# Kernel tuning notes

Measured on AMD Instinct MI355X. Metric: run time of the kernel, lower is better.

Reference implementation:

```python
import jax, jax.numpy as jnp
import numpy as np

B, KLEN, QLEN = 4, 512, 64
KDIM = QDIM = ADIM = 512
H = 4
DK = ADIM // H


def setup_inputs() -> dict:
    key = jax.random.key(0)
    ks = jax.random.split(key, 8)
    inp = {}
    inp["key"] = jax.random.normal(ks[0], (B, KLEN, KDIM), jnp.float32)
    inp["query"] = jax.random.normal(ks[1], (B, QLEN, QDIM), jnp.float32)
    inp["mask"] = jax.random.randint(ks[2], (B, QLEN, KLEN), 0, 2, jnp.int32)
    # nn.Linear default init scale ~ 1/sqrt(fan_in)
    inp["w_key_w"] = jax.random.normal(ks[3], (ADIM, KDIM), jnp.float32) / np.sqrt(KDIM)
    inp["w_key_b"] = jnp.zeros((ADIM,), jnp.float32)
    inp["w_query_w"] = jax.random.normal(ks[4], (ADIM, QDIM), jnp.float32) / np.sqrt(QDIM)
    # weight-normed v: weight = g * v / ||v||_row, g initialized to sqrt(1/adim)
    inp["v_v"] = jax.random.normal(ks[5], (H, ADIM), jnp.float32) / np.sqrt(ADIM)
    inp["v_g"] = jnp.full((H, 1), np.sqrt(1.0 / ADIM), jnp.float32)
    inp["r"] = jnp.array([-4.0], jnp.float32)  # init_r
    return inp


def reference(key, query, mask, w_key_w, w_key_b, w_query_w, v_v, v_g, r):
    bs, klen, _ = key.shape
    qlen = query.shape[1]
    # key projection -> [B, H, klen, d_k]
    k = (jnp.einsum('bkd,ad->bka', key, w_key_w) + w_key_b)
    k = k.reshape(bs, klen, H, DK).transpose(0, 2, 1, 3)
    # query projection (no bias) -> [B, H, qlen, d_k]
    q = jnp.einsum('bqd,ad->bqa', query, w_query_w)
    q = q.reshape(bs, qlen, H, DK).transpose(0, 2, 1, 3)
    # additive energy: relu(k + q) over [B, H, qlen, klen, d_k]
    e5 = jax.nn.relu(k[:, :, None, :, :] + q[:, :, :, None, :])
    # weight-normed v linear mixes heads: Wv[n, h, d]
    Wv = (v_g * v_v / jnp.linalg.norm(v_v, axis=1, keepdims=True)).reshape(H, H, DK)
    e = jnp.einsum('bhqkd,nhd->bnqk', e5, Wv)
    e = e + r[0]
    neg_inf = jnp.finfo(e.dtype).min
    m = jnp.broadcast_to(mask[:, None, :, :], e.shape)  # [B, H, qlen, klen]
    e = jnp.where(m == 0, neg_inf, e)
    return e
```

## Files before the change

### kernel.cpp

```cpp
#include <hip/hip_runtime.h>
#include <math.h>

#define KLEN 512
#define QLEN 64
#define ADIM 512
#define BATCH 4
#define NH 4

typedef __attribute__((ext_vector_type(8))) short bf16x8;
typedef __attribute__((ext_vector_type(4))) float f32x4;
typedef _Float16 f16;
typedef __attribute__((ext_vector_type(2))) _Float16 f16x2;

__device__ __forceinline__ f16x2 u2h(unsigned int u) {
  union { unsigned int u; f16x2 h; } v; v.u = u; return v.h;
}

__device__ __forceinline__ short4 pack4(float4 x) {
  union { unsigned int u[2]; short4 s; } o;
  o.u[0] = __builtin_amdgcn_perm(__float_as_uint(x.y), __float_as_uint(x.x), 0x07060302);
  o.u[1] = __builtin_amdgcn_perm(__float_as_uint(x.w), __float_as_uint(x.z), 0x07060302);
  return o.s;
}

__global__ __launch_bounds__(512) void proj_mfma(
    const float* __restrict__ key, const float* __restrict__ query,
    const float* __restrict__ wk, const float* __restrict__ bk,
    const float* __restrict__ wq,
    const float* __restrict__ v_v, const float* __restrict__ v_g,
    f16* __restrict__ Kp, f16* __restrict__ Qp, f16* __restrict__ Wn) {
  __shared__ short At[2][64 * 40];
  __shared__ short Wt[2][64 * 40];

  const int bid = blockIdx.x;
  const int tid = threadIdx.x;

  if (bid == 288) {
    __shared__ float wred[512];
    for (int h = 0; h < NH; ++h) {
      float v0 = v_v[h * ADIM + tid];
      wred[tid] = v0 * v0;
      __syncthreads();
      for (int s2 = 256; s2 > 0; s2 >>= 1) {
        if (tid < s2) wred[tid] += wred[tid + s2];
        __syncthreads();
      }
      float scale = v_g[h] / sqrtf(wred[0]);
      Wn[h * ADIM + tid] = (f16)(v0 * scale);
      __syncthreads();
    }
    return;
  }

  const float *A, *W, *bias;
  f16* C;
  int m0, a0;
  if (bid < 256) {
    A = key; W = wk; bias = bk; C = Kp;
    m0 = (bid >> 3) * 64; a0 = (bid & 7) * 64;
  } else {
    const int t = bid - 256;
    A = query; W = wq; bias = nullptr; C = Qp;
    m0 = (t >> 3) * 64; a0 = (t & 7) * 64;
  }

  const int w = tid >> 6;
  const int wr = w >> 2;
  const int wc = w & 3;
  const int lane = tid & 63;
  const int lr = lane & 15, hi = lane >> 4;
  const int srow = tid >> 3;
  const int scol = (tid & 7) * 4;

  const float* Arow = &A[(size_t)(m0 + srow) * ADIM + scol];
  const float* Wrow = &W[(size_t)(a0 + srow) * ADIM + scol];

  f32x4 acc0 = {0.f, 0.f, 0.f, 0.f};
  f32x4 acc1 = {0.f, 0.f, 0.f, 0.f};

  {
    float4 fa = *(const float4*)&Arow[0];
    float4 fw = *(const float4*)&Wrow[0];
    *(short4*)&At[0][srow * 40 + scol] = pack4(fa);
    *(short4*)&Wt[0][srow * 40 + scol] = pack4(fw);
  }
  __syncthreads();

  for (int c = 0; c < 16; ++c) {
    float4 na, nw;
    if (c < 15) {
      na = *(const float4*)&Arow[(c + 1) * 32];
      nw = *(const float4*)&Wrow[(c + 1) * 32];
    }
    const short* Ab = At[c & 1];
    const short* Wb = Wt[c & 1];
    bf16x8 af0 = *(const bf16x8*)&Ab[(wr * 32 + lr) * 40 + hi * 8];
    bf16x8 af1 = *(const bf16x8*)&Ab[(wr * 32 + 16 + lr) * 40 + hi * 8];
    bf16x8 wf  = *(const bf16x8*)&Wb[(wc * 16 + lr) * 40 + hi * 8];
    acc0 = __builtin_amdgcn_mfma_f32_16x16x32_bf16(af0, wf, acc0, 0, 0, 0);
    acc1 = __builtin_amdgcn_mfma_f32_16x16x32_bf16(af1, wf, acc1, 0, 0, 0);
    if (c < 15) {
      *(short4*)&At[(c + 1) & 1][srow * 40 + scol] = pack4(na);
      *(short4*)&Wt[(c + 1) & 1][srow * 40 + scol] = pack4(nw);
    }
    __syncthreads();
  }

  const int ccol = a0 + wc * 16 + lr;
  const float bv = bias ? bias[ccol] : 0.f;
#pragma unroll
  for (int i = 0; i < 4; ++i) {
    const int crow0 = m0 + wr * 32 + hi * 4 + i;
    C[(size_t)crow0 * ADIM + ccol] = (f16)(acc0[i] + bv);
    C[(size_t)(crow0 + 16) * ADIM + ccol] = (f16)(acc1[i] + bv);
  }
}

__global__ __launch_bounds__(256) void energy_kernel(
    const f16* __restrict__ Kp, const f16* __restrict__ Qp,
    const f16* __restrict__ Wn, const int* __restrict__ mask,
    const float* __restrict__ r, float* __restrict__ out) {
  __shared__ f16 Kl[16 * 520];
  __shared__ f16 Ql[16 * 520];
  __shared__ float Red[2][1280];

  const int b = blockIdx.z;
  const int q0 = blockIdx.y * 16;
  const int kl0 = blockIdx.x * 16;
  const int tid = threadIdx.x;
  const int wave = tid >> 6;
  const int lane = tid & 63;
  const int klg = lane & 7;
  const int qg = lane >> 3;

  const float rv = r[0];

  const unsigned short* Kb = (const unsigned short*)(Kp + ((size_t)b * KLEN + kl0) * ADIM);
  const unsigned short* Qb = (const unsigned short*)(Qp + ((size_t)b * QLEN + q0) * ADIM);

  const unsigned int* Wd = (const unsigned int*)Wn;
  uint4 wreg = *(const uint4*)&Wd[(lane >> 4) * 256 + wave * 64 + (lane & 15) * 4];

#pragma unroll
  for (int j = 0; j < 4; ++j) {
    const int u = tid + 256 * j;
    const int row = u >> 6, c8 = (u & 63) * 8;
    *(uint4*)&Kl[row * 520 + c8] = *(const uint4*)&Kb[row * ADIM + c8];
    *(uint4*)&Ql[row * 520 + c8] = *(const uint4*)&Qb[row * ADIM + c8];
  }
  __syncthreads();

  float acc[2][2][4] = {};
  const int abase = wave * 128;

#pragma unroll
  for (int s = 0; s < 16; ++s) {
    const int off = abase + s * 8;
    uint4 ka = *(const uint4*)&Kl[klg * 520 + off];
    uint4 kb = *(const uint4*)&Kl[(klg + 8) * 520 + off];
    uint4 qa = *(const uint4*)&Ql[qg * 520 + off];
    uint4 qb = *(const uint4*)&Ql[(qg + 8) * 520 + off];
    unsigned wdw[4][4];
#pragma unroll
    for (int n = 0; n < 4; ++n) {
      wdw[n][0] = (unsigned)__builtin_amdgcn_readlane((int)wreg.x, n * 16 + s);
      wdw[n][1] = (unsigned)__builtin_amdgcn_readlane((int)wreg.y, n * 16 + s);
      wdw[n][2] = (unsigned)__builtin_amdgcn_readlane((int)wreg.z, n * 16 + s);
      wdw[n][3] = (unsigned)__builtin_amdgcn_readlane((int)wreg.w, n * 16 + s);
    }
    unsigned ks[2][4] = {{ka.x, ka.y, ka.z, ka.w}, {kb.x, kb.y, kb.z, kb.w}};
    unsigned qs[2][4] = {{qa.x, qa.y, qa.z, qa.w}, {qb.x, qb.y, qb.z, qb.w}};
#pragma unroll
    for (int j = 0; j < 4; ++j) {
      const f16x2 wv0 = u2h(wdw[0][j]), wv1 = u2h(wdw[1][j]);
      const f16x2 wv2 = u2h(wdw[2][j]), wv3 = u2h(wdw[3][j]);
#pragma unroll
      for (int ki = 0; ki < 2; ++ki) {
        const f16x2 kv = u2h(ks[ki][j]);
#pragma unroll
        for (int qi = 0; qi < 2; ++qi) {
          f16x2 sum = kv + u2h(qs[qi][j]);
          f16x2 rl = __builtin_elementwise_max(sum, (f16x2)(_Float16)0);
          acc[ki][qi][0] = __builtin_amdgcn_fdot2(rl, wv0, acc[ki][qi][0], false);
          acc[ki][qi][1] = __builtin_amdgcn_fdot2(rl, wv1, acc[ki][qi][1], false);
          acc[ki][qi][2] = __builtin_amdgcn_fdot2(rl, wv2, acc[ki][qi][2], false);
          acc[ki][qi][3] = __builtin_amdgcn_fdot2(rl, wv3, acc[ki][qi][3], false);
        }
      }
    }
  }

  const int half = wave & 1;
  if (wave < 2) {
#pragma unroll
    for (int ki = 0; ki < 2; ++ki)
#pragma unroll
      for (int qi = 0; qi < 2; ++qi) {
        const int cell = (qg + 8 * qi) * 16 + klg + 8 * ki;
#pragma unroll
        for (int n = 0; n < 4; ++n) Red[half][cell * 5 + n] = acc[ki][qi][n];
      }
  }
  __syncthreads();
  if (wave >= 2) {
#pragma unroll
    for (int ki = 0; ki < 2; ++ki)
#pragma unroll
      for (int qi = 0; qi < 2; ++qi) {
        const int cell = (qg + 8 * qi) * 16 + klg + 8 * ki;
#pragma unroll
        for (int n = 0; n < 4; ++n) Red[half][cell * 5 + n] += acc[ki][qi][n];
      }
  }
  __syncthreads();

  const float NEG_BIG = __uint_as_float(0xFF7F0000u);
  const int n = tid >> 6;
  const int q = (tid >> 2) & 15;
  const int klb = (tid & 3) * 4;
  const int4 mv = *(const int4*)&mask[((size_t)b * QLEN + q0 + q) * KLEN + kl0 + klb];
  const int mm[4] = {mv.x, mv.y, mv.z, mv.w};
  float4 o;
  float* op = &o.x;
#pragma unroll
  for (int t = 0; t < 4; ++t) {
    const int cell = q * 16 + klb + t;
    float v = Red[0][cell * 5 + n] + Red[1][cell * 5 + n] + rv;
    op[t] = mm[t] ? v : NEG_BIG;
  }
  *(float4*)&out[(((size_t)b * NH + n) * QLEN + q0 + q) * KLEN + kl0 + klb] = o;
}

extern "C" void kernel_launch(void* const* d_in, const int* in_sizes, int n_in,
                              void* d_out, int out_size, void* d_ws, size_t ws_size,
                              hipStream_t stream) {
  const float* key   = (const float*)d_in[0];
  const float* query = (const float*)d_in[1];
  const int*   mask  = (const int*)d_in[2];
  const float* wk    = (const float*)d_in[3];
  const float* bk    = (const float*)d_in[4];
  const float* wq    = (const float*)d_in[5];
  const float* v_v   = (const float*)d_in[6];
  const float* v_g   = (const float*)d_in[7];
  const float* r     = (const float*)d_in[8];
  float* out = (float*)d_out;

  f16* Kp = (f16*)d_ws;
  f16* Qp = Kp + (size_t)2048 * 512;
  f16* Wn = Qp + (size_t)256 * 512;

  hipLaunchKernelGGL(proj_mfma, dim3(289), dim3(512), 0, stream,
                     key, query, wk, bk, wq, v_v, v_g, Kp, Qp, Wn);
  hipLaunchKernelGGL(energy_kernel, dim3(32, 4, 4), dim3(256), 0, stream,
                     Kp, Qp, Wn, mask, r, out);
}
```

Baseline: 25.98 us.

## Retile projection GEMM to 64x32 tiles with 64-wide K steps and 256 threads

The projection kernel now uses 64x32 output tiles with 4 waves per block instead of 64x64 with 8 waves, which doubles the grid to 577 blocks. Each K step covers 64 elements (two MFMAs per step) over 8 iterations instead of 32 over 16. The aim is to fill more CUs and halve the number of barriers and loop iterations. In exchange, each activation tile is loaded from global memory twice as many times across blocks, and each thread keeps more prefetched data in registers.

```diff
diff --git a/kernel.cpp b/kernel.cpp
--- a/kernel.cpp
+++ b/kernel.cpp
@@ -23,30 +23,32 @@
   return o.s;
 }
 
-__global__ __launch_bounds__(512) void proj_mfma(
+__global__ __launch_bounds__(256) void proj_mfma(
     const float* __restrict__ key, const float* __restrict__ query,
     const float* __restrict__ wk, const float* __restrict__ bk,
     const float* __restrict__ wq,
     const float* __restrict__ v_v, const float* __restrict__ v_g,
     f16* __restrict__ Kp, f16* __restrict__ Qp, f16* __restrict__ Wn) {
-  __shared__ short At[2][64 * 40];
-  __shared__ short Wt[2][64 * 40];
+  __shared__ short At[2][64 * 72];
+  __shared__ short Wt[2][32 * 72];
 
   const int bid = blockIdx.x;
   const int tid = threadIdx.x;
 
-  if (bid == 288) {
-    __shared__ float wred[512];
+  if (bid == 576) {
+    __shared__ float wred[256];
     for (int h = 0; h < NH; ++h) {
       float v0 = v_v[h * ADIM + tid];
-      wred[tid] = v0 * v0;
+      float v1 = v_v[h * ADIM + tid + 256];
+      wred[tid] = v0 * v0 + v1 * v1;
       __syncthreads();
-      for (int s2 = 256; s2 > 0; s2 >>= 1) {
+      for (int s2 = 128; s2 > 0; s2 >>= 1) {
         if (tid < s2) wred[tid] += wred[tid + s2];
         __syncthreads();
       }
       float scale = v_g[h] / sqrtf(wred[0]);
       Wn[h * ADIM + tid] = (f16)(v0 * scale);
+      Wn[h * ADIM + tid + 256] = (f16)(v1 * scale);
       __syncthreads();
     }
     return;
@@ -55,53 +57,75 @@
   const float *A, *W, *bias;
   f16* C;
   int m0, a0;
-  if (bid < 256) {
+  if (bid < 512) {
     A = key; W = wk; bias = bk; C = Kp;
-    m0 = (bid >> 3) * 64; a0 = (bid & 7) * 64;
+    m0 = (bid >> 4) * 64; a0 = (bid & 15) * 32;
   } else {
-    const int t = bid - 256;
+    const int t = bid - 512;
     A = query; W = wq; bias = nullptr; C = Qp;
-    m0 = (t >> 3) * 64; a0 = (t & 7) * 64;
-  }
-
-  const int w = tid >> 6;
-  const int wr = w >> 2;
-  const int wc = w & 3;
+    m0 = (t >> 4) * 64; a0 = (t & 15) * 32;
+  }
+
+  const int wave = tid >> 6;
+  const int wr = wave >> 1;
+  const int wc = wave & 1;
   const int lane = tid & 63;
   const int lr = lane & 15, hi = lane >> 4;
-  const int srow = tid >> 3;
-  const int scol = (tid & 7) * 4;
-
-  const float* Arow = &A[(size_t)(m0 + srow) * ADIM + scol];
-  const float* Wrow = &W[(size_t)(a0 + srow) * ADIM + scol];
+
+  const int arow = tid >> 2, acol = (tid & 3) * 16;
+  const int wrow = tid >> 3, wcol = (tid & 7) * 8;
+
+  const float* Ab = &A[(size_t)(m0 + arow) * ADIM + acol];
+  const float* Wb = &W[(size_t)(a0 + wrow) * ADIM + wcol];
 
   f32x4 acc0 = {0.f, 0.f, 0.f, 0.f};
   f32x4 acc1 = {0.f, 0.f, 0.f, 0.f};
 
+  float4 a4[4], w4[2];
+#pragma unroll
+  for (int j = 0; j < 4; ++j) a4[j] = *(const float4*)&Ab[j * 4];
+#pragma unroll
+  for (int j = 0; j < 2; ++j) w4[j] = *(const float4*)&Wb[j * 4];
   {
-    float4 fa = *(const float4*)&Arow[0];
-    float4 fw = *(const float4*)&Wrow[0];
-    *(short4*)&At[0][srow * 40 + scol] = pack4(fa);
-    *(short4*)&Wt[0][srow * 40 + scol] = pack4(fw);
-  }
-  __syncthreads();
-
-  for (int c = 0; c < 16; ++c) {
-    float4 na, nw;
-    if (c < 15) {
-      na = *(const float4*)&Arow[(c + 1) * 32];
-      nw = *(const float4*)&Wrow[(c + 1) * 32];
-    }
-    const short* Ab = At[c & 1];
-    const short* Wb = Wt[c & 1];
-    bf16x8 af0 = *(const bf16x8*)&Ab[(wr * 32 + lr) * 40 + hi * 8];
-    bf16x8 af1 = *(const bf16x8*)&Ab[(wr * 32 + 16 + lr) * 40 + hi * 8];
-    bf16x8 wf  = *(const bf16x8*)&Wb[(wc * 16 + lr) * 40 + hi * 8];
-    acc0 = __builtin_amdgcn_mfma_f32_16x16x32_bf16(af0, wf, acc0, 0, 0, 0);
-    acc1 = __builtin_amdgcn_mfma_f32_16x16x32_bf16(af1, wf, acc1, 0, 0, 0);
-    if (c < 15) {
-      *(short4*)&At[(c + 1) & 1][srow * 40 + scol] = pack4(na);
-      *(short4*)&Wt[(c + 1) & 1][srow * 40 + scol] = pack4(nw);
+    short4 p0 = pack4(a4[0]), p1 = pack4(a4[1]), p2 = pack4(a4[2]), p3 = pack4(a4[3]);
+    *(short4*)&At[0][arow * 72 + acol] = p0;
+    *(short4*)&At[0][arow * 72 + acol + 4] = p1;
+    *(short4*)&At[0][arow * 72 + acol + 8] = p2;
+    *(short4*)&At[0][arow * 72 + acol + 12] = p3;
+    short4 q0 = pack4(w4[0]), q1 = pack4(w4[1]);
+    *(short4*)&Wt[0][wrow * 72 + wcol] = q0;
+    *(short4*)&Wt[0][wrow * 72 + wcol + 4] = q1;
+  }
+  __syncthreads();
+
+  for (int c = 0; c < 8; ++c) {
+    if (c < 7) {
+      const int base = (c + 1) * 64;
+#pragma unroll
+      for (int j = 0; j < 4; ++j) a4[j] = *(const float4*)&Ab[base + j * 4];
+#pragma unroll
+      for (int j = 0; j < 2; ++j) w4[j] = *(const float4*)&Wb[base + j * 4];
+    }
+    const short* Abuf = At[c & 1];
+    const short* Wbuf = Wt[c & 1];
+#pragma unroll
+    for (int kk = 0; kk < 2; ++kk) {
+      bf16x8 wf = *(const bf16x8*)&Wbuf[(wc * 16 + lr) * 72 + kk * 32 + hi * 8];
+      bf16x8 af0 = *(const bf16x8*)&Abuf[(wr * 32 + lr) * 72 + kk * 32 + hi * 8];
+      bf16x8 af1 = *(const bf16x8*)&Abuf[(wr * 32 + 16 + lr) * 72 + kk * 32 + hi * 8];
+      acc0 = __builtin_amdgcn_mfma_f32_16x16x32_bf16(af0, wf, acc0, 0, 0, 0);
+      acc1 = __builtin_amdgcn_mfma_f32_16x16x32_bf16(af1, wf, acc1, 0, 0, 0);
+    }
+    if (c < 7) {
+      const int nb = (c + 1) & 1;
+      short4 p0 = pack4(a4[0]), p1 = pack4(a4[1]), p2 = pack4(a4[2]), p3 = pack4(a4[3]);
+      *(short4*)&At[nb][arow * 72 + acol] = p0;
+      *(short4*)&At[nb][arow * 72 + acol + 4] = p1;
+      *(short4*)&At[nb][arow * 72 + acol + 8] = p2;
+      *(short4*)&At[nb][arow * 72 + acol + 12] = p3;
+      short4 q0 = pack4(w4[0]), q1 = pack4(w4[1]);
+      *(short4*)&Wt[nb][wrow * 72 + wcol] = q0;
+      *(short4*)&Wt[nb][wrow * 72 + wcol + 4] = q1;
     }
     __syncthreads();
   }
@@ -110,9 +134,9 @@
   const float bv = bias ? bias[ccol] : 0.f;
 #pragma unroll
   for (int i = 0; i < 4; ++i) {
-    const int crow0 = m0 + wr * 32 + hi * 4 + i;
-    C[(size_t)crow0 * ADIM + ccol] = (f16)(acc0[i] + bv);
-    C[(size_t)(crow0 + 16) * ADIM + ccol] = (f16)(acc1[i] + bv);
+    const int crow = m0 + wr * 32 + hi * 4 + i;
+    C[(size_t)crow * ADIM + ccol] = (f16)(acc0[i] + bv);
+    C[(size_t)(crow + 16) * ADIM + ccol] = (f16)(acc1[i] + bv);
   }
 }
 
@@ -249,7 +273,7 @@
   f16* Qp = Kp + (size_t)2048 * 512;
   f16* Wn = Qp + (size_t)256 * 512;
 
-  hipLaunchKernelGGL(proj_mfma, dim3(289), dim3(512), 0, stream,
+  hipLaunchKernelGGL(proj_mfma, dim3(577), dim3(256), 0, stream,
                      key, query, wk, bk, wq, v_v, v_g, Kp, Qp, Wn);
   hipLaunchKernelGGL(energy_kernel, dim3(32, 4, 4), dim3(256), 0, stream,
                      Kp, Qp, Wn, mask, r, out);
```

Result: slower. 27.94 us (+7.5%).
